# Kernel tuning notes

Hardware: AMD Instinct MI355X
Metric: run time of the kernel (lower is better)

## Reference

```python
import jax, jax.numpy as jnp
import numpy as np

N_NODES = 100000
N_EDGES = 3200000
IN_C, HID_C, OUT_C = 64, 128, 64


def gcn_conv(x, src, dst, W, b, n):
    """PyG GCNConv: h = x @ W; out[d] += norm(e) * h[s]; norm = deg^-1/2[s]*deg^-1/2[d].
    src/dst already include self-loops."""
    h = x @ W  # [N, out_c]
    deg = jax.ops.segment_sum(jnp.ones_like(dst, dtype=h.dtype), dst, num_segments=n)
    dinv = jnp.where(deg > 0, jax.lax.rsqrt(deg), 0.0)
    norm = dinv[src] * dinv[dst]  # [E]
    msg = h[src] * norm[:, None]  # [E, out_c] -- dominant memory traffic
    return jax.ops.segment_sum(msg, dst, num_segments=n) + b


def setup_inputs() -> dict:
    key = jax.random.key(0)
    k1, k2, k3, k4 = jax.random.split(key, 4)
    x = jax.random.normal(k1, (N_NODES, IN_C), dtype=jnp.float32)
    edge_index = jax.random.randint(k2, (2, N_EDGES), 0, N_NODES, dtype=jnp.int64)
    W1 = jax.random.normal(k3, (IN_C, HID_C), dtype=jnp.float32) / np.sqrt(IN_C)
    b1 = jnp.zeros((HID_C,), dtype=jnp.float32)
    W2 = jax.random.normal(k4, (HID_C, OUT_C), dtype=jnp.float32) / np.sqrt(HID_C)
    b2 = jnp.zeros((OUT_C,), dtype=jnp.float32)
    return {"x": x, "edge_index": edge_index, "W1": W1, "b1": b1, "W2": W2, "b2": b2}


def reference(x, edge_index, W1, b1, W2, b2):
    n = x.shape[0]
    loops = jnp.arange(n, dtype=edge_index.dtype)  # self-loops, as PyG GCNConv adds
    src = jnp.concatenate([edge_index[0], loops])
    dst = jnp.concatenate([edge_index[1], loops])
    h = gcn_conv(x, src, dst, W1, b1, n)
    h = jax.nn.relu(h)
    out = gcn_conv(h, src, dst, W2, b2, n)
    return out
```

## Files before the change

### kernel.cpp

```cpp
#include <hip/hip_runtime.h>
#include <math.h>


#define IN_C 64
#define HID_C 128
#define OUT_C 64
#define BSHIFT 9
#define BW (1 << BSHIFT)
#define NPB 512
#define CAP 24576
#define CH_MAX 6272

typedef __attribute__((ext_vector_type(8))) short bf16x8;
typedef __attribute__((ext_vector_type(4))) float f32x4;
typedef __attribute__((ext_vector_type(2))) float v2f;

__device__ __forceinline__ unsigned short f2bf(float f) {
  unsigned u = __float_as_uint(f);
  return (unsigned short)((u + 0x7FFF + ((u >> 16) & 1)) >> 16);
}
__device__ __forceinline__ v2f cvt2(unsigned u) {
  v2f r;
  r.x = __uint_as_float(u << 16);
  r.y = __uint_as_float(u & 0xFFFF0000u);
  return r;
}
__device__ __forceinline__ unsigned pack2(v2f v) {
  return ((unsigned)f2bf(v.y) << 16) | f2bf(v.x);
}


__global__ __launch_bounds__(256) void k_build(const int* __restrict__ ei, int e, int n,
    int nb, int* __restrict__ gcnt, unsigned* __restrict__ ebuf,
    const float* __restrict__ W1, const float* __restrict__ W2,
    unsigned short* __restrict__ Wt1, unsigned short* __restrict__ Wt2,
    unsigned short* __restrict__ xs_zero, unsigned short* __restrict__ h2s_zero) {
  const int t = threadIdx.x;
  if (blockIdx.x >= NPB) {
    int bb = blockIdx.x - NPB;
    if (bb == 32) {
      if (t < 64) { xs_zero[t] = 0; h2s_zero[t] = 0; }
      return;
    }
    int i = bb * 256 + t;
    if (i < IN_C * HID_C) {
      int k = i >> 7, c = i & (HID_C - 1);
      Wt1[c * IN_C + k] = f2bf(W1[i]);
    }
    if (i < HID_C * OUT_C) {
      int k = i >> 6, c = i & (OUT_C - 1);
      Wt2[c * HID_C + k] = f2bf(W2[i]);
    }
    return;
  }
  __shared__ unsigned lpay[CH_MAX];
  __shared__ unsigned char lbuck[CH_MAX];
  __shared__ int lh[256];
  __shared__ int lbase[256];
  __shared__ int lcur[256];
  __shared__ int sflag;
  if (t == 0) sflag = 0;
  __syncthreads();
  const int chunk = (e + NPB - 1) / NPB;
  const int lo = blockIdx.x * chunk;
  const int hi = min(lo + chunk, e);
  {
    int lim = min(hi, lo + 512);
    int f = 0;
    for (int i = lo + t; i < lim; i += 256)
      if (ei[2 * i + 1] != 0) f = 1;
    if (f) sflag = 1;
  }
  __syncthreads();
  const int f = sflag;
  for (int sub = lo; sub < hi; sub += CH_MAX) {
    const int shi = min(sub + CH_MAX, hi);
    const int mm = shi - sub;
    for (int i = t; i < nb; i += 256) lh[i] = 0;
    __syncthreads();
    for (int i = sub + t; i < shi; i += 256) {
      int s, d;
      if (f) {
        s = __builtin_nontemporal_load(&ei[i]);
        d = __builtin_nontemporal_load(&ei[e + i]);
      } else {
        s = (int)__builtin_nontemporal_load(&((const long long*)ei)[i]);
        d = (int)__builtin_nontemporal_load(&((const long long*)ei)[e + i]);
      }
      s = min(max(s, 0), n - 1);
      d = min(max(d, 0), n - 1);
      int bk = d >> BSHIFT;
      lpay[i - sub] = ((unsigned)(d & (BW - 1)) << 23) | (unsigned)s;
      lbuck[i - sub] = (unsigned char)bk;
      atomicAdd(&lh[bk], 1);
    }
    __syncthreads();
    for (int i = t; i < nb; i += 256) {
      int c = lh[i];
      lbase[i] = c ? atomicAdd(&gcnt[i], c) : 0;
      lcur[i] = 0;
    }
    __syncthreads();
    for (int i = t; i < mm; i += 256) {
      int bk = lbuck[i];
      int slot = lbase[bk] + atomicAdd(&lcur[bk], 1);
      if (slot < CAP) ebuf[(size_t)bk * CAP + slot] = lpay[i];
    }
    __syncthreads();
  }
}


__global__ __launch_bounds__(1024) void k_finalize(const unsigned* __restrict__ ebuf,
    const int* __restrict__ gcnt, const float* __restrict__ x,
    unsigned short* __restrict__ xs, int n, int nb,
    int* __restrict__ row_ptr, float* __restrict__ dinv, int* __restrict__ col) {
  __shared__ int sc[256];
  __shared__ int ldeg[BW];
  __shared__ int lofs[BW];
  __shared__ int lcur[BW];
  __shared__ float sdv[BW];
  __shared__ int wsum[256];
  const int b = blockIdx.x;
  const int t = threadIdx.x;
  const int T = 1024;
  int cnt = 0, nodes = 0;
  if (t < nb) {
    cnt = min(gcnt[t], CAP);
    nodes = min(BW, n - t * BW);
  }
  if (t < 256) sc[t] = cnt + nodes;
  __syncthreads();
  for (int off = 1; off < 256; off <<= 1) {
    int vc = 0;
    if (t < 256 && t >= off) vc = sc[t - off];
    __syncthreads();
    if (t < 256) sc[t] += vc;
    __syncthreads();
  }
  const int cntb = min(gcnt[b], CAP);
  const int eb = b * CAP;
  const int ee = eb + cntb;
  const int cb = (b == 0) ? 0 : sc[b - 1];
  const int lo = b * BW;
  const int nn = min(BW, n - lo);
  for (int k = t; k < BW; k += T) ldeg[k] = 0;
  __syncthreads();
  for (int k = t; k < nn; k += T) ldeg[k] = 1;
  __syncthreads();
  for (int j = eb + t; j < ee; j += T) {
    int dl = (int)(ebuf[j] >> 23);
    atomicAdd(&ldeg[dl], 1);
  }
  __syncthreads();
  int p0 = 0, p1 = 0;
  if (t < 256) {
    p0 = ldeg[2 * t]; p1 = ldeg[2 * t + 1];
    wsum[t] = p0 + p1;
  }
  __syncthreads();
  for (int off = 1; off < 256; off <<= 1) {
    int v = 0;
    if (t < 256 && t >= off) v = wsum[t - off];
    __syncthreads();
    if (t < 256) wsum[t] += v;
    __syncthreads();
  }
  if (t < 256) {
    int pb = (t == 0) ? 0 : wsum[t - 1];
    lofs[2 * t] = pb;
    lofs[2 * t + 1] = pb + p0;
  }
  __syncthreads();
  for (int k = t; k < nn; k += T) {
    int base = cb + lofs[k];
    float dv = rsqrtf((float)ldeg[k]);
    row_ptr[lo + k] = base;
    dinv[lo + k] = dv;
    sdv[k] = dv;
    col[base] = lo + k;
    lcur[k] = lofs[k] + 1;
  }
  if (b == nb - 1 && t == 0) row_ptr[n] = sc[nb - 1];
  __syncthreads();
  for (int j = eb + t; j < ee; j += T) {
    unsigned pk = ebuf[j];
    int s = (int)(pk & 0x7FFFFF);
    int dl = (int)(pk >> 23);
    int p = atomicAdd(&lcur[dl], 1);
    col[cb + p] = s;
  }
  const float4* x4 = (const float4*)x;
  for (int idx = t; idx < nn * 16; idx += T) {
    int row = idx >> 4, q = idx & 15;
    float sc2 = sdv[row];
    float4 v = x4[(size_t)(lo + row) * 16 + q];
    ushort4 o;
    o.x = f2bf(v.x * sc2); o.y = f2bf(v.y * sc2);
    o.z = f2bf(v.z * sc2); o.w = f2bf(v.w * sc2);
    ((ushort4*)xs)[(size_t)(lo + row) * 16 + q] = o;
  }
}


__device__ __forceinline__ void agg_row(const char* __restrict__ fb,
    const int* __restrict__ col, int beg, int end, int es, unsigned coff, int n,
    v2f& a0, v2f& a1, v2f& a2, v2f& a3) {
  const int rem = end - beg - es;
  const int c = (rem > 0) ? ((rem + 7) >> 3) : 0;
  const int last = end - 1;
  const unsigned zrow = ((unsigned)n << 7) | coff;
  for (int g = 0; g < c; g += 4) {
    int j0 = beg + es + 8 * g;
    int i0 = __builtin_nontemporal_load(&col[j0]);
    int i1 = __builtin_nontemporal_load(&col[min(j0 + 8, last)]);
    int i2 = __builtin_nontemporal_load(&col[min(j0 + 16, last)]);
    int i3 = __builtin_nontemporal_load(&col[min(j0 + 24, last)]);
    unsigned o0 = ((unsigned)i0 << 7) | coff;
    unsigned o1 = (g + 1 >= c) ? zrow : (((unsigned)i1 << 7) | coff);
    unsigned o2 = (g + 2 >= c) ? zrow : (((unsigned)i2 << 7) | coff);
    unsigned o3 = (g + 3 >= c) ? zrow : (((unsigned)i3 << 7) | coff);
    uint4 u0 = *(const uint4*)(fb + o0);
    uint4 u1 = *(const uint4*)(fb + o1);
    uint4 u2 = *(const uint4*)(fb + o2);
    uint4 u3 = *(const uint4*)(fb + o3);
    a0 += cvt2(u0.x) + cvt2(u1.x) + cvt2(u2.x) + cvt2(u3.x);
    a1 += cvt2(u0.y) + cvt2(u1.y) + cvt2(u2.y) + cvt2(u3.y);
    a2 += cvt2(u0.z) + cvt2(u1.z) + cvt2(u2.z) + cvt2(u3.z);
    a3 += cvt2(u0.w) + cvt2(u1.w) + cvt2(u2.w) + cvt2(u3.w);
  }
#pragma unroll
  for (int off = 8; off <= 32; off <<= 1) {
    v2f o0, o1, o2, o3;
    o0.x = __shfl_xor(a0.x, off); o0.y = __shfl_xor(a0.y, off);
    o1.x = __shfl_xor(a1.x, off); o1.y = __shfl_xor(a1.y, off);
    o2.x = __shfl_xor(a2.x, off); o2.y = __shfl_xor(a2.y, off);
    o3.x = __shfl_xor(a3.x, off); o3.y = __shfl_xor(a3.y, off);
    a0 += o0; a1 += o1; a2 += o2; a3 += o3;
  }
}


__global__ __launch_bounds__(256) void k_agg2(const unsigned short* __restrict__ feat,
    const int* __restrict__ row_ptr, const int* __restrict__ col,
    const float* __restrict__ dinv, const float* __restrict__ bias,
    float* __restrict__ out, int n) {
  const int wid = threadIdx.x >> 6;
  const int lane = threadIdx.x & 63;
  const int es = lane >> 3;
  const int c8 = lane & 7;
  const int d = blockIdx.x * 4 + wid;
  if (d >= n) return;
  const int beg = row_ptr[d], end = row_ptr[d + 1];
  v2f a0 = {0.f, 0.f}, a1 = {0.f, 0.f}, a2 = {0.f, 0.f}, a3 = {0.f, 0.f};
  agg_row((const char*)feat, col, beg, end, es, (unsigned)c8 * 16u, n,
          a0, a1, a2, a3);
  if (es == 0) {
    float sc = dinv[d];
    v2f vs = {sc, sc};
    a0 *= vs; a1 *= vs; a2 *= vs; a3 *= vs;
    const v2f* b2v = (const v2f*)bias;
    a0 += b2v[c8 * 4 + 0]; a1 += b2v[c8 * 4 + 1];
    a2 += b2v[c8 * 4 + 2]; a3 += b2v[c8 * 4 + 3];
    float4* o4 = (float4*)out;
    o4[(size_t)d * 16 + c8 * 2]     = make_float4(a0.x, a0.y, a1.x, a1.y);
    o4[(size_t)d * 16 + c8 * 2 + 1] = make_float4(a2.x, a2.y, a3.x, a3.y);
  }
}


__global__ __launch_bounds__(512) void k_aggmlp(const unsigned short* __restrict__ feat,
    const int* __restrict__ row_ptr, const int* __restrict__ col,
    const float* __restrict__ dinv, const float* __restrict__ b1,
    const unsigned short* __restrict__ Wt1, const unsigned short* __restrict__ Wt2,
    unsigned short* __restrict__ h2s, int n) {
  __shared__ __align__(16) unsigned short sA1[16][72];
  __shared__ __align__(16) unsigned short sH[16][136];
  const int wv = threadIdx.x >> 6;
  const int lane = threadIdx.x & 63;
  const int es = lane >> 3;
  const int c8 = lane & 7;
  const int r0 = blockIdx.x * 16;
  const unsigned coff = (unsigned)c8 * 16u;
  for (int rr = 0; rr < 2; ++rr) {
    const int d = r0 + wv * 2 + rr;
    if (d < n) {
      const int beg = row_ptr[d], end = row_ptr[d + 1];
      v2f a0 = {0.f, 0.f}, a1 = {0.f, 0.f}, a2 = {0.f, 0.f}, a3 = {0.f, 0.f};
      agg_row((const char*)feat, col, beg, end, es, coff, n, a0, a1, a2, a3);
      if (es == 0) {
        float sc = dinv[d];
        v2f vs = {sc, sc};
        a0 *= vs; a1 *= vs; a2 *= vs; a3 *= vs;
        uint4 o;
        o.x = pack2(a0); o.y = pack2(a1); o.z = pack2(a2); o.w = pack2(a3);
        *(uint4*)&sA1[wv * 2 + rr][c8 * 8] = o;
      }
    } else if (es == 0) {
      uint4 z = {0u, 0u, 0u, 0u};
      *(uint4*)&sA1[wv * 2 + rr][c8 * 8] = z;
    }
  }
  __syncthreads();
  const int m = lane & 15;
  const int q = lane >> 4;
  f32x4 acc0 = {0.f, 0.f, 0.f, 0.f};
#pragma unroll
  for (int kt = 0; kt < IN_C; kt += 32) {
    bf16x8 a = *(const bf16x8*)&sA1[m][kt + q * 8];
    bf16x8 p = *(const bf16x8*)&Wt1[(size_t)(wv * 16 + m) * IN_C + kt + q * 8];
    acc0 = __builtin_amdgcn_mfma_f32_16x16x32_bf16(a, p, acc0, 0, 0, 0);
  }
  float dv[4];
#pragma unroll
  for (int i = 0; i < 4; i++) dv[i] = dinv[min(r0 + q * 4 + i, n - 1)];
  {
    int c = wv * 16 + m;
    float bv = b1[c];
#pragma unroll
    for (int i = 0; i < 4; i++)
      sH[q * 4 + i][c] = f2bf(fmaxf(acc0[i] + bv, 0.f) * dv[i]);
  }
  __syncthreads();
  if (wv < 4) {
    f32x4 acc = {0.f, 0.f, 0.f, 0.f};
#pragma unroll
    for (int kt = 0; kt < HID_C; kt += 32) {
      bf16x8 a = *(const bf16x8*)&sH[m][kt + q * 8];
      bf16x8 p = *(const bf16x8*)&Wt2[(size_t)(wv * 16 + m) * HID_C + kt + q * 8];
      acc = __builtin_amdgcn_mfma_f32_16x16x32_bf16(a, p, acc, 0, 0, 0);
    }
    int c = wv * 16 + m;
#pragma unroll
    for (int i = 0; i < 4; i++) {
      int row = r0 + q * 4 + i;
      if (row < n) h2s[(size_t)row * OUT_C + c] = f2bf(acc[i]);
    }
  }
}


extern "C" void kernel_launch(void* const* d_in, const int* in_sizes, int n_in,
                              void* d_out, int out_size, void* d_ws, size_t ws_size,
                              hipStream_t stream) {
  const float* x  = (const float*)d_in[0];
  const int*   ei = (const int*)d_in[1];
  const float* W1 = (const float*)d_in[2];
  const float* b1 = (const float*)d_in[3];
  const float* W2 = (const float*)d_in[4];
  const float* b2 = (const float*)d_in[5];
  float* out = (float*)d_out;

  const int n = in_sizes[0] / IN_C;
  const int e = in_sizes[1] / 2;
  const int nb = (n + BW - 1) >> BSHIFT;

  char* p = (char*)d_ws;
  auto alloc = [&](size_t bytes) {
    char* r = p;
    p += (bytes + 255) & ~(size_t)255;
    return r;
  };
  int*   gcnt       = (int*)alloc((size_t)nb * 4);
  int*   row_ptr    = (int*)alloc((size_t)(n + 1) * 4);
  float* dinv       = (float*)alloc((size_t)n * 4);
  int*   col        = (int*)alloc((size_t)(e + n) * 4);
  unsigned* ebuf    = (unsigned*)alloc((size_t)nb * CAP * 4);
  unsigned short* xs  = (unsigned short*)alloc((size_t)(n + 1) * IN_C * 2);
  unsigned short* h2s = (unsigned short*)alloc((size_t)(n + 1) * OUT_C * 2);
  unsigned short* Wt1 = (unsigned short*)alloc((size_t)IN_C * HID_C * 2);
  unsigned short* Wt2 = (unsigned short*)alloc((size_t)HID_C * OUT_C * 2);

  hipMemsetAsync(gcnt, 0, (size_t)nb * 4, stream);

  k_build<<<NPB + 33, 256, 0, stream>>>(ei, e, n, nb, gcnt, ebuf, W1, W2, Wt1, Wt2,
      xs + (size_t)n * IN_C, h2s + (size_t)n * OUT_C);
  k_finalize<<<nb, 1024, 0, stream>>>(ebuf, gcnt, x, xs, n, nb, row_ptr, dinv, col);

  k_aggmlp<<<(n + 15) / 16, 512, 0, stream>>>(xs, row_ptr, col, dinv, b1, Wt1, Wt2, h2s, n);
  k_agg2<<<(n + 3) / 4, 256, 0, stream>>>(h2s, row_ptr, col, dinv, b2, out, n);
}
```

Measured before the change: 290.4 us.

## Merge all stages into one persistent cooperative kernel with grid syncs

Replaces the four separate kernels (build, finalize, aggregate+MLP, aggregate) with a single persistent kernel, launched cooperatively, that uses grid-wide syncs between phases. Layer-1 aggregation now writes an intermediate A1 buffer and a separate phase runs the MLP on 64-row tiles. This aims to remove launch gaps and tail effects between kernels. In exchange it adds grid barriers, an extra global round trip for A1, fewer resident threads per phase, and a multi-launch fallback when cooperative launch is unavailable.

```diff
diff --git a/kernel.cpp b/kernel.cpp
--- a/kernel.cpp
+++ b/kernel.cpp
@@ -1,5 +1,8 @@
 #include <hip/hip_runtime.h>
+#include <hip/hip_cooperative_groups.h>
 #include <math.h>
+
+namespace cg = cooperative_groups;
 
 
 #define IN_C 64
@@ -7,9 +10,11 @@
 #define OUT_C 64
 #define BSHIFT 9
 #define BW (1 << BSHIFT)
-#define NPB 512
+#define MAXBLK 512
+#define NTHR 1024
 #define CAP 24576
 #define CH_MAX 6272
+#define SMEM_BYTES 35840
 
 typedef __attribute__((ext_vector_type(8))) short bf16x8;
 typedef __attribute__((ext_vector_type(4))) float f32x4;
@@ -27,179 +32,6 @@
 }
 __device__ __forceinline__ unsigned pack2(v2f v) {
   return ((unsigned)f2bf(v.y) << 16) | f2bf(v.x);
-}
-
-
-__global__ __launch_bounds__(256) void k_build(const int* __restrict__ ei, int e, int n,
-    int nb, int* __restrict__ gcnt, unsigned* __restrict__ ebuf,
-    const float* __restrict__ W1, const float* __restrict__ W2,
-    unsigned short* __restrict__ Wt1, unsigned short* __restrict__ Wt2,
-    unsigned short* __restrict__ xs_zero, unsigned short* __restrict__ h2s_zero) {
-  const int t = threadIdx.x;
-  if (blockIdx.x >= NPB) {
-    int bb = blockIdx.x - NPB;
-    if (bb == 32) {
-      if (t < 64) { xs_zero[t] = 0; h2s_zero[t] = 0; }
-      return;
-    }
-    int i = bb * 256 + t;
-    if (i < IN_C * HID_C) {
-      int k = i >> 7, c = i & (HID_C - 1);
-      Wt1[c * IN_C + k] = f2bf(W1[i]);
-    }
-    if (i < HID_C * OUT_C) {
-      int k = i >> 6, c = i & (OUT_C - 1);
-      Wt2[c * HID_C + k] = f2bf(W2[i]);
-    }
-    return;
-  }
-  __shared__ unsigned lpay[CH_MAX];
-  __shared__ unsigned char lbuck[CH_MAX];
-  __shared__ int lh[256];
-  __shared__ int lbase[256];
-  __shared__ int lcur[256];
-  __shared__ int sflag;
-  if (t == 0) sflag = 0;
-  __syncthreads();
-  const int chunk = (e + NPB - 1) / NPB;
-  const int lo = blockIdx.x * chunk;
-  const int hi = min(lo + chunk, e);
-  {
-    int lim = min(hi, lo + 512);
-    int f = 0;
-    for (int i = lo + t; i < lim; i += 256)
-      if (ei[2 * i + 1] != 0) f = 1;
-    if (f) sflag = 1;
-  }
-  __syncthreads();
-  const int f = sflag;
-  for (int sub = lo; sub < hi; sub += CH_MAX) {
-    const int shi = min(sub + CH_MAX, hi);
-    const int mm = shi - sub;
-    for (int i = t; i < nb; i += 256) lh[i] = 0;
-    __syncthreads();
-    for (int i = sub + t; i < shi; i += 256) {
-      int s, d;
-      if (f) {
-        s = __builtin_nontemporal_load(&ei[i]);
-        d = __builtin_nontemporal_load(&ei[e + i]);
-      } else {
-        s = (int)__builtin_nontemporal_load(&((const long long*)ei)[i]);
-        d = (int)__builtin_nontemporal_load(&((const long long*)ei)[e + i]);
-      }
-      s = min(max(s, 0), n - 1);
-      d = min(max(d, 0), n - 1);
-      int bk = d >> BSHIFT;
-      lpay[i - sub] = ((unsigned)(d & (BW - 1)) << 23) | (unsigned)s;
-      lbuck[i - sub] = (unsigned char)bk;
-      atomicAdd(&lh[bk], 1);
-    }
-    __syncthreads();
-    for (int i = t; i < nb; i += 256) {
-      int c = lh[i];
-      lbase[i] = c ? atomicAdd(&gcnt[i], c) : 0;
-      lcur[i] = 0;
-    }
-    __syncthreads();
-    for (int i = t; i < mm; i += 256) {
-      int bk = lbuck[i];
-      int slot = lbase[bk] + atomicAdd(&lcur[bk], 1);
-      if (slot < CAP) ebuf[(size_t)bk * CAP + slot] = lpay[i];
-    }
-    __syncthreads();
-  }
-}
-
-
-__global__ __launch_bounds__(1024) void k_finalize(const unsigned* __restrict__ ebuf,
-    const int* __restrict__ gcnt, const float* __restrict__ x,
-    unsigned short* __restrict__ xs, int n, int nb,
-    int* __restrict__ row_ptr, float* __restrict__ dinv, int* __restrict__ col) {
-  __shared__ int sc[256];
-  __shared__ int ldeg[BW];
-  __shared__ int lofs[BW];
-  __shared__ int lcur[BW];
-  __shared__ float sdv[BW];
-  __shared__ int wsum[256];
-  const int b = blockIdx.x;
-  const int t = threadIdx.x;
-  const int T = 1024;
-  int cnt = 0, nodes = 0;
-  if (t < nb) {
-    cnt = min(gcnt[t], CAP);
-    nodes = min(BW, n - t * BW);
-  }
-  if (t < 256) sc[t] = cnt + nodes;
-  __syncthreads();
-  for (int off = 1; off < 256; off <<= 1) {
-    int vc = 0;
-    if (t < 256 && t >= off) vc = sc[t - off];
-    __syncthreads();
-    if (t < 256) sc[t] += vc;
-    __syncthreads();
-  }
-  const int cntb = min(gcnt[b], CAP);
-  const int eb = b * CAP;
-  const int ee = eb + cntb;
-  const int cb = (b == 0) ? 0 : sc[b - 1];
-  const int lo = b * BW;
-  const int nn = min(BW, n - lo);
-  for (int k = t; k < BW; k += T) ldeg[k] = 0;
-  __syncthreads();
-  for (int k = t; k < nn; k += T) ldeg[k] = 1;
-  __syncthreads();
-  for (int j = eb + t; j < ee; j += T) {
-    int dl = (int)(ebuf[j] >> 23);
-    atomicAdd(&ldeg[dl], 1);
-  }
-  __syncthreads();
-  int p0 = 0, p1 = 0;
-  if (t < 256) {
-    p0 = ldeg[2 * t]; p1 = ldeg[2 * t + 1];
-    wsum[t] = p0 + p1;
-  }
-  __syncthreads();
-  for (int off = 1; off < 256; off <<= 1) {
-    int v = 0;
-    if (t < 256 && t >= off) v = wsum[t - off];
-    __syncthreads();
-    if (t < 256) wsum[t] += v;
-    __syncthreads();
-  }
-  if (t < 256) {
-    int pb = (t == 0) ? 0 : wsum[t - 1];
-    lofs[2 * t] = pb;
-    lofs[2 * t + 1] = pb + p0;
-  }
-  __syncthreads();
-  for (int k = t; k < nn; k += T) {
-    int base = cb + lofs[k];
-    float dv = rsqrtf((float)ldeg[k]);
-    row_ptr[lo + k] = base;
-    dinv[lo + k] = dv;
-    sdv[k] = dv;
-    col[base] = lo + k;
-    lcur[k] = lofs[k] + 1;
-  }
-  if (b == nb - 1 && t == 0) row_ptr[n] = sc[nb - 1];
-  __syncthreads();
-  for (int j = eb + t; j < ee; j += T) {
-    unsigned pk = ebuf[j];
-    int s = (int)(pk & 0x7FFFFF);
-    int dl = (int)(pk >> 23);
-    int p = atomicAdd(&lcur[dl], 1);
-    col[cb + p] = s;
-  }
-  const float4* x4 = (const float4*)x;
-  for (int idx = t; idx < nn * 16; idx += T) {
-    int row = idx >> 4, q = idx & 15;
-    float sc2 = sdv[row];
-    float4 v = x4[(size_t)(lo + row) * 16 + q];
-    ushort4 o;
-    o.x = f2bf(v.x * sc2); o.y = f2bf(v.y * sc2);
-    o.z = f2bf(v.z * sc2); o.w = f2bf(v.w * sc2);
-    ((ushort4*)xs)[(size_t)(lo + row) * 16 + q] = o;
-  }
 }
 
 
@@ -216,10 +48,10 @@
     int i1 = __builtin_nontemporal_load(&col[min(j0 + 8, last)]);
     int i2 = __builtin_nontemporal_load(&col[min(j0 + 16, last)]);
     int i3 = __builtin_nontemporal_load(&col[min(j0 + 24, last)]);
-    unsigned o0 = ((unsigned)i0 << 7) | coff;
-    unsigned o1 = (g + 1 >= c) ? zrow : (((unsigned)i1 << 7) | coff);
-    unsigned o2 = (g + 2 >= c) ? zrow : (((unsigned)i2 << 7) | coff);
-    unsigned o3 = (g + 3 >= c) ? zrow : (((unsigned)i3 << 7) | coff);
+    unsigned o0 = min(((unsigned)i0 << 7) | coff, zrow);
+    unsigned o1 = (g + 1 >= c) ? zrow : min(((unsigned)i1 << 7) | coff, zrow);
+    unsigned o2 = (g + 2 >= c) ? zrow : min(((unsigned)i2 << 7) | coff, zrow);
+    unsigned o3 = (g + 3 >= c) ? zrow : min(((unsigned)i3 << 7) | coff, zrow);
     uint4 u0 = *(const uint4*)(fb + o0);
     uint4 u1 = *(const uint4*)(fb + o1);
     uint4 u2 = *(const uint4*)(fb + o2);
@@ -241,100 +73,291 @@
 }
 
 
-__global__ __launch_bounds__(256) void k_agg2(const unsigned short* __restrict__ feat,
-    const int* __restrict__ row_ptr, const int* __restrict__ col,
-    const float* __restrict__ dinv, const float* __restrict__ bias,
-    float* __restrict__ out, int n) {
-  const int wid = threadIdx.x >> 6;
-  const int lane = threadIdx.x & 63;
-  const int es = lane >> 3;
-  const int c8 = lane & 7;
-  const int d = blockIdx.x * 4 + wid;
-  if (d >= n) return;
-  const int beg = row_ptr[d], end = row_ptr[d + 1];
-  v2f a0 = {0.f, 0.f}, a1 = {0.f, 0.f}, a2 = {0.f, 0.f}, a3 = {0.f, 0.f};
-  agg_row((const char*)feat, col, beg, end, es, (unsigned)c8 * 16u, n,
-          a0, a1, a2, a3);
-  if (es == 0) {
-    float sc = dinv[d];
-    v2f vs = {sc, sc};
-    a0 *= vs; a1 *= vs; a2 *= vs; a3 *= vs;
-    const v2f* b2v = (const v2f*)bias;
-    a0 += b2v[c8 * 4 + 0]; a1 += b2v[c8 * 4 + 1];
-    a2 += b2v[c8 * 4 + 2]; a3 += b2v[c8 * 4 + 3];
-    float4* o4 = (float4*)out;
-    o4[(size_t)d * 16 + c8 * 2]     = make_float4(a0.x, a0.y, a1.x, a1.y);
-    o4[(size_t)d * 16 + c8 * 2 + 1] = make_float4(a2.x, a2.y, a3.x, a3.y);
-  }
-}
-
-
-__global__ __launch_bounds__(512) void k_aggmlp(const unsigned short* __restrict__ feat,
-    const int* __restrict__ row_ptr, const int* __restrict__ col,
-    const float* __restrict__ dinv, const float* __restrict__ b1,
-    const unsigned short* __restrict__ Wt1, const unsigned short* __restrict__ Wt2,
-    unsigned short* __restrict__ h2s, int n) {
-  __shared__ __align__(16) unsigned short sA1[16][72];
-  __shared__ __align__(16) unsigned short sH[16][136];
-  const int wv = threadIdx.x >> 6;
-  const int lane = threadIdx.x & 63;
-  const int es = lane >> 3;
-  const int c8 = lane & 7;
-  const int r0 = blockIdx.x * 16;
-  const unsigned coff = (unsigned)c8 * 16u;
-  for (int rr = 0; rr < 2; ++rr) {
-    const int d = r0 + wv * 2 + rr;
-    if (d < n) {
-      const int beg = row_ptr[d], end = row_ptr[d + 1];
+__global__ __launch_bounds__(NTHR, 8) void k_all(
+    const float* __restrict__ x, const int* __restrict__ ei,
+    const float* __restrict__ W1, const float* __restrict__ b1v,
+    const float* __restrict__ W2, const float* __restrict__ b2v,
+    float* __restrict__ out, int e, int n, int nb,
+    int* __restrict__ gcnt, unsigned* __restrict__ ebuf,
+    int* __restrict__ row_ptr, float* __restrict__ dinv,
+    int* __restrict__ col, int col_cap,
+    unsigned short* __restrict__ xs, unsigned short* __restrict__ A1,
+    unsigned short* __restrict__ h2s,
+    unsigned short* __restrict__ Wt1, unsigned short* __restrict__ Wt2,
+    int plo, int phi, int coop) {
+  __shared__ __align__(16) char smem[SMEM_BYTES];
+  const int bid = blockIdx.x;
+  const int gd = gridDim.x;
+  const int t = threadIdx.x;
+
+  if (plo <= 0 && 0 < phi) {
+    if (bid == 0) {
+      for (int i = t; i < IN_C * HID_C; i += NTHR) {
+        int k = i >> 7, c = i & (HID_C - 1);
+        Wt1[c * IN_C + k] = f2bf(W1[i]);
+      }
+    } else if (bid == 1) {
+      for (int i = t; i < HID_C * OUT_C; i += NTHR) {
+        int k = i >> 6, c = i & (OUT_C - 1);
+        Wt2[c * HID_C + k] = f2bf(W2[i]);
+      }
+    } else if (bid == 2) {
+      if (t < IN_C) xs[(size_t)n * IN_C + t] = 0;
+      if (t < OUT_C) h2s[(size_t)n * OUT_C + t] = 0;
+    }
+  }
+
+  if (plo <= 1 && 1 < phi) {
+    unsigned* lpay = (unsigned*)smem;
+    unsigned char* lbuck = (unsigned char*)(lpay + CH_MAX);
+    int* lh = (int*)(lbuck + CH_MAX);
+    int* lbase = lh + 256;
+    int* lcur = lbase + 256;
+    int* sflag = lcur + 256;
+    if (t == 0) *sflag = 0;
+    for (int i = t; i < 256; i += NTHR) lh[i] = 0;
+    __syncthreads();
+    const int chunk = (e + gd - 1) / gd;
+    const int lo = bid * chunk;
+    const int hi = min(lo + chunk, e);
+    {
+      int lim = min(hi, lo + 1024);
+      int fl = 0;
+      for (int i = lo + t; i < lim; i += NTHR)
+        if (ei[2 * i + 1] != 0) fl = 1;
+      if (fl) *sflag = 1;
+    }
+    __syncthreads();
+    const int f = *sflag;
+    const int nsub = (chunk + CH_MAX - 1) / CH_MAX;
+    for (int su = 0; su < nsub; ++su) {
+      const int sub = lo + su * CH_MAX;
+      const int shi = min(sub + CH_MAX, hi);
+      const int mm = max(shi - sub, 0);
+      for (int i = sub + t; i < shi; i += NTHR) {
+        int s, d;
+        if (f) {
+          s = __builtin_nontemporal_load(&ei[i]);
+          d = __builtin_nontemporal_load(&ei[e + i]);
+        } else {
+          s = (int)__builtin_nontemporal_load(&((const long long*)ei)[i]);
+          d = (int)__builtin_nontemporal_load(&((const long long*)ei)[e + i]);
+        }
+        s = min(max(s, 0), n - 1);
+        d = min(max(d, 0), n - 1);
+        int bk = d >> BSHIFT;
+        lpay[i - sub] = ((unsigned)(d & (BW - 1)) << 23) | (unsigned)s;
+        lbuck[i - sub] = (unsigned char)bk;
+        atomicAdd(&lh[bk], 1);
+      }
+      __syncthreads();
+      for (int i = t; i < nb; i += NTHR) {
+        int c = lh[i];
+        lbase[i] = c ? atomicAdd(&gcnt[i], c) : 0;
+        lh[i] = 0;
+        lcur[i] = 0;
+      }
+      __syncthreads();
+      for (int i = t; i < mm; i += NTHR) {
+        int bk = lbuck[i];
+        int slot = lbase[bk] + atomicAdd(&lcur[bk], 1);
+        if (slot < CAP) ebuf[(size_t)bk * CAP + slot] = lpay[i];
+      }
+      __syncthreads();
+    }
+  }
+  if (coop && 2 < phi) cg::this_grid().sync();
+
+  if (plo <= 2 && 2 < phi && bid < nb) {
+    int* sc = (int*)smem;
+    int* ldeg = sc + 256;
+    int* lofs = ldeg + BW;
+    int* lcur = lofs + BW;
+    float* sdv = (float*)(lcur + BW);
+    int* wsum = (int*)(sdv + BW);
+    const int b = bid;
+    int pc = 0;
+    if (t < nb) {
+      int cnt = min(__hip_atomic_load(&gcnt[t], __ATOMIC_RELAXED, __HIP_MEMORY_SCOPE_AGENT), CAP);
+      int nodes = min(BW, n - t * BW);
+      pc = (cnt + nodes + 31) & ~31;
+    }
+    if (t < 256) sc[t] = pc;
+    __syncthreads();
+    for (int off = 1; off < 256; off <<= 1) {
+      int vc = 0;
+      if (t < 256 && t >= off) vc = sc[t - off];
+      __syncthreads();
+      if (t < 256) sc[t] += vc;
+      __syncthreads();
+    }
+    const int cntb = min(__hip_atomic_load(&gcnt[b], __ATOMIC_RELAXED, __HIP_MEMORY_SCOPE_AGENT), CAP);
+    const int eb = b * CAP;
+    const int ee = eb + cntb;
+    const int cb = (b == 0) ? 0 : sc[b - 1];
+    const int lo = b * BW;
+    const int nn = min(BW, n - lo);
+    for (int k = t; k < BW; k += NTHR) ldeg[k] = 0;
+    __syncthreads();
+    for (int k = t; k < nn; k += NTHR) ldeg[k] = 1;
+    __syncthreads();
+    for (int j = eb + t; j < ee; j += NTHR) {
+      unsigned pk = __hip_atomic_load(&ebuf[j], __ATOMIC_RELAXED, __HIP_MEMORY_SCOPE_AGENT);
+      atomicAdd(&ldeg[(int)(pk >> 23)], 1);
+    }
+    __syncthreads();
+    int p0 = 0, p1 = 0;
+    if (t < 256) {
+      p0 = ldeg[2 * t]; p1 = ldeg[2 * t + 1];
+      wsum[t] = p0 + p1;
+    }
+    __syncthreads();
+    for (int off = 1; off < 256; off <<= 1) {
+      int v = 0;
+      if (t < 256 && t >= off) v = wsum[t - off];
+      __syncthreads();
+      if (t < 256) wsum[t] += v;
+      __syncthreads();
+    }
+    if (t < 256) {
+      int pb = (t == 0) ? 0 : wsum[t - 1];
+      lofs[2 * t] = pb;
+      lofs[2 * t + 1] = pb + p0;
+    }
+    __syncthreads();
+    for (int k = t; k < nn; k += NTHR) {
+      int base = cb + lofs[k];
+      float dv = rsqrtf((float)ldeg[k]);
+      row_ptr[lo + k] = base;
+      dinv[lo + k] = dv;
+      sdv[k] = dv;
+      if (base >= 0 && base < col_cap) col[base] = lo + k;
+      lcur[k] = lofs[k] + 1;
+    }
+    if (b == nb - 1 && t == 0) row_ptr[n] = cb + cntb + nn;
+    __syncthreads();
+    for (int j = eb + t; j < ee; j += NTHR) {
+      unsigned pk = __hip_atomic_load(&ebuf[j], __ATOMIC_RELAXED, __HIP_MEMORY_SCOPE_AGENT);
+      int s = (int)(pk & 0x7FFFFF);
+      int dl = (int)(pk >> 23);
+      int p = atomicAdd(&lcur[dl], 1);
+      int idx = cb + p;
+      if (idx >= 0 && idx < col_cap) col[idx] = s;
+    }
+    const float4* x4 = (const float4*)x;
+    for (int idx = t; idx < nn * 16; idx += NTHR) {
+      int row = idx >> 4, q = idx & 15;
+      float sc2 = sdv[row];
+      float4 v = x4[(size_t)(lo + row) * 16 + q];
+      ushort4 o;
+      o.x = f2bf(v.x * sc2); o.y = f2bf(v.y * sc2);
+      o.z = f2bf(v.z * sc2); o.w = f2bf(v.w * sc2);
+      ((ushort4*)xs)[(size_t)(lo + row) * 16 + q] = o;
+    }
+  }
+  if (coop && 3 < phi) cg::this_grid().sync();
+
+  if (plo <= 3 && 3 < phi) {
+    const int wv = t >> 6;
+    const int lane = t & 63;
+    const int es = lane >> 3;
+    const int c8 = lane & 7;
+    const unsigned coff = (unsigned)c8 * 16u;
+    for (int d = bid * 16 + wv; d < n; d += gd * 16) {
+      int beg = row_ptr[d], end = row_ptr[d + 1];
+      beg = max(beg, 0); end = min(end, col_cap); end = max(end, beg);
       v2f a0 = {0.f, 0.f}, a1 = {0.f, 0.f}, a2 = {0.f, 0.f}, a3 = {0.f, 0.f};
-      agg_row((const char*)feat, col, beg, end, es, coff, n, a0, a1, a2, a3);
+      agg_row((const char*)xs, col, beg, end, es, coff, n, a0, a1, a2, a3);
       if (es == 0) {
-        float sc = dinv[d];
-        v2f vs = {sc, sc};
+        float scv = dinv[d];
+        v2f vs = {scv, scv};
         a0 *= vs; a1 *= vs; a2 *= vs; a3 *= vs;
         uint4 o;
         o.x = pack2(a0); o.y = pack2(a1); o.z = pack2(a2); o.w = pack2(a3);
-        *(uint4*)&sA1[wv * 2 + rr][c8 * 8] = o;
-      }
-    } else if (es == 0) {
-      uint4 z = {0u, 0u, 0u, 0u};
-      *(uint4*)&sA1[wv * 2 + rr][c8 * 8] = z;
-    }
-  }
-  __syncthreads();
-  const int m = lane & 15;
-  const int q = lane >> 4;
-  f32x4 acc0 = {0.f, 0.f, 0.f, 0.f};
-#pragma unroll
-  for (int kt = 0; kt < IN_C; kt += 32) {
-    bf16x8 a = *(const bf16x8*)&sA1[m][kt + q * 8];
-    bf16x8 p = *(const bf16x8*)&Wt1[(size_t)(wv * 16 + m) * IN_C + kt + q * 8];
-    acc0 = __builtin_amdgcn_mfma_f32_16x16x32_bf16(a, p, acc0, 0, 0, 0);
-  }
-  float dv[4];
-#pragma unroll
-  for (int i = 0; i < 4; i++) dv[i] = dinv[min(r0 + q * 4 + i, n - 1)];
-  {
-    int c = wv * 16 + m;
-    float bv = b1[c];
-#pragma unroll
-    for (int i = 0; i < 4; i++)
-      sH[q * 4 + i][c] = f2bf(fmaxf(acc0[i] + bv, 0.f) * dv[i]);
-  }
-  __syncthreads();
-  if (wv < 4) {
-    f32x4 acc = {0.f, 0.f, 0.f, 0.f};
-#pragma unroll
-    for (int kt = 0; kt < HID_C; kt += 32) {
-      bf16x8 a = *(const bf16x8*)&sH[m][kt + q * 8];
-      bf16x8 p = *(const bf16x8*)&Wt2[(size_t)(wv * 16 + m) * HID_C + kt + q * 8];
-      acc = __builtin_amdgcn_mfma_f32_16x16x32_bf16(a, p, acc, 0, 0, 0);
-    }
-    int c = wv * 16 + m;
-#pragma unroll
-    for (int i = 0; i < 4; i++) {
-      int row = r0 + q * 4 + i;
-      if (row < n) h2s[(size_t)row * OUT_C + c] = f2bf(acc[i]);
+        ((uint4*)A1)[(size_t)d * 8 + c8] = o;
+      }
+    }
+  }
+  if (coop && 4 < phi) cg::this_grid().sync();
+
+  if (plo <= 4 && 4 < phi) {
+    typedef unsigned short ush;
+    ush (*sH)[136] = (ush(*)[136])smem;
+    const int wv = t >> 6;
+    const int team = wv >> 2;
+    const int tw = wv & 3;
+    const int lane = t & 63;
+    const int m = lane & 15;
+    const int q = lane >> 4;
+    const int nt64 = (n + 63) >> 6;
+    for (int tile = bid; tile < nt64; tile += gd) {
+      const int r0t = tile * 64 + team * 16;
+      const int ra = min(r0t + m, n - 1);
+      f32x4 acc0 = {0.f, 0.f, 0.f, 0.f}, acc1 = {0.f, 0.f, 0.f, 0.f};
+#pragma unroll
+      for (int kt = 0; kt < IN_C; kt += 32) {
+        bf16x8 a  = *(const bf16x8*)&A1[(size_t)ra * IN_C + kt + q * 8];
+        bf16x8 p  = *(const bf16x8*)&Wt1[(size_t)(tw * 16 + m) * IN_C + kt + q * 8];
+        bf16x8 p2 = *(const bf16x8*)&Wt1[(size_t)((tw + 4) * 16 + m) * IN_C + kt + q * 8];
+        acc0 = __builtin_amdgcn_mfma_f32_16x16x32_bf16(a, p, acc0, 0, 0, 0);
+        acc1 = __builtin_amdgcn_mfma_f32_16x16x32_bf16(a, p2, acc1, 0, 0, 0);
+      }
+      float dv[4];
+#pragma unroll
+      for (int i = 0; i < 4; i++) dv[i] = dinv[min(r0t + q * 4 + i, n - 1)];
+      {
+        int c = tw * 16 + m;
+        float bv = b1v[c];
+#pragma unroll
+        for (int i = 0; i < 4; i++)
+          sH[team * 16 + q * 4 + i][c] = f2bf(fmaxf(acc0[i] + bv, 0.f) * dv[i]);
+        c = (tw + 4) * 16 + m;
+        bv = b1v[c];
+#pragma unroll
+        for (int i = 0; i < 4; i++)
+          sH[team * 16 + q * 4 + i][c] = f2bf(fmaxf(acc1[i] + bv, 0.f) * dv[i]);
+      }
+      __syncthreads();
+      f32x4 acc = {0.f, 0.f, 0.f, 0.f};
+#pragma unroll
+      for (int kt = 0; kt < HID_C; kt += 32) {
+        bf16x8 a = *(const bf16x8*)&sH[team * 16 + m][kt + q * 8];
+        bf16x8 p = *(const bf16x8*)&Wt2[(size_t)(tw * 16 + m) * HID_C + kt + q * 8];
+        acc = __builtin_amdgcn_mfma_f32_16x16x32_bf16(a, p, acc, 0, 0, 0);
+      }
+      int c = tw * 16 + m;
+#pragma unroll
+      for (int i = 0; i < 4; i++) {
+        int row = r0t + q * 4 + i;
+        if (row < n) h2s[(size_t)row * OUT_C + c] = f2bf(acc[i]);
+      }
+      __syncthreads();
+    }
+  }
+  if (coop && 5 < phi) cg::this_grid().sync();
+
+  if (plo <= 5 && 5 < phi) {
+    const int wv = t >> 6;
+    const int lane = t & 63;
+    const int es = lane >> 3;
+    const int c8 = lane & 7;
+    const unsigned coff = (unsigned)c8 * 16u;
+    const v2f* b2p = (const v2f*)b2v;
+    for (int d = bid * 16 + wv; d < n; d += gd * 16) {
+      int beg = row_ptr[d], end = row_ptr[d + 1];
+      beg = max(beg, 0); end = min(end, col_cap); end = max(end, beg);
+      v2f a0 = {0.f, 0.f}, a1 = {0.f, 0.f}, a2 = {0.f, 0.f}, a3 = {0.f, 0.f};
+      agg_row((const char*)h2s, col, beg, end, es, coff, n, a0, a1, a2, a3);
+      if (es == 0) {
+        float scv = dinv[d];
+        v2f vs = {scv, scv};
+        a0 *= vs; a1 *= vs; a2 *= vs; a3 *= vs;
+        a0 += b2p[c8 * 4 + 0]; a1 += b2p[c8 * 4 + 1];
+        a2 += b2p[c8 * 4 + 2]; a3 += b2p[c8 * 4 + 3];
+        float4* o4 = (float4*)out;
+        o4[(size_t)d * 16 + c8 * 2]     = make_float4(a0.x, a0.y, a1.x, a1.y);
+        o4[(size_t)d * 16 + c8 * 2 + 1] = make_float4(a2.x, a2.y, a3.x, a3.y);
+      }
     }
   }
 }
@@ -355,28 +378,63 @@
   const int e = in_sizes[1] / 2;
   const int nb = (n + BW - 1) >> BSHIFT;
 
+  static int s_nblk = -1;
+  static int s_coop = 0;
+  if (s_nblk < 0) {
+    int dev = 0;
+    hipGetDevice(&dev);
+    hipDeviceProp_t props;
+    hipGetDeviceProperties(&props, dev);
+    int maxb = 0;
+    hipOccupancyMaxActiveBlocksPerMultiprocessor(&maxb, (const void*)k_all, NTHR, 0);
+    if (maxb < 1) maxb = 1;
+    long cap = (long)maxb * props.multiProcessorCount;
+    s_nblk = (int)(cap < MAXBLK ? cap : MAXBLK);
+    if (s_nblk < 1) s_nblk = 256;
+    s_coop = props.cooperativeLaunch ? 1 : 0;
+    if (s_nblk < nb) s_coop = 0;
+  }
+
   char* p = (char*)d_ws;
   auto alloc = [&](size_t bytes) {
     char* r = p;
     p += (bytes + 255) & ~(size_t)255;
     return r;
   };
-  int*   gcnt       = (int*)alloc((size_t)nb * 4);
+  const int col_cap = e + n + 32 * nb + 64;
+  int*   gcnt       = (int*)alloc((size_t)256 * 4);
   int*   row_ptr    = (int*)alloc((size_t)(n + 1) * 4);
   float* dinv       = (float*)alloc((size_t)n * 4);
-  int*   col        = (int*)alloc((size_t)(e + n) * 4);
+  int*   col        = (int*)alloc((size_t)col_cap * 4);
   unsigned* ebuf    = (unsigned*)alloc((size_t)nb * CAP * 4);
   unsigned short* xs  = (unsigned short*)alloc((size_t)(n + 1) * IN_C * 2);
+  unsigned short* A1  = (unsigned short*)alloc((size_t)n * IN_C * 2);
   unsigned short* h2s = (unsigned short*)alloc((size_t)(n + 1) * OUT_C * 2);
   unsigned short* Wt1 = (unsigned short*)alloc((size_t)IN_C * HID_C * 2);
   unsigned short* Wt2 = (unsigned short*)alloc((size_t)HID_C * OUT_C * 2);
 
-  hipMemsetAsync(gcnt, 0, (size_t)nb * 4, stream);
-
-  k_build<<<NPB + 33, 256, 0, stream>>>(ei, e, n, nb, gcnt, ebuf, W1, W2, Wt1, Wt2,
-      xs + (size_t)n * IN_C, h2s + (size_t)n * OUT_C);
-  k_finalize<<<nb, 1024, 0, stream>>>(ebuf, gcnt, x, xs, n, nb, row_ptr, dinv, col);
-
-  k_aggmlp<<<(n + 15) / 16, 512, 0, stream>>>(xs, row_ptr, col, dinv, b1, Wt1, Wt2, h2s, n);
-  k_agg2<<<(n + 3) / 4, 256, 0, stream>>>(h2s, row_ptr, col, dinv, b2, out, n);
-}
+  hipMemsetAsync(gcnt, 0, (size_t)256 * 4, stream);
+
+  if (s_coop) {
+    int plo = 0, phi = 6, coop = 1;
+    void* args[] = {
+      (void*)&x, (void*)&ei, (void*)&W1, (void*)&b1, (void*)&W2, (void*)&b2,
+      (void*)&out, (void*)&e, (void*)&n, (void*)&nb,
+      (void*)&gcnt, (void*)&ebuf, (void*)&row_ptr, (void*)&dinv,
+      (void*)&col, (void*)&col_cap, (void*)&xs, (void*)&A1, (void*)&h2s,
+      (void*)&Wt1, (void*)&Wt2, (void*)&plo, (void*)&phi, (void*)&coop};
+    hipLaunchCooperativeKernel((const void*)k_all, dim3(s_nblk), dim3(NTHR),
+                               args, 0, stream);
+  } else {
+    k_all<<<s_nblk, NTHR, 0, stream>>>(x, ei, W1, b1, W2, b2, out, e, n, nb,
+        gcnt, ebuf, row_ptr, dinv, col, col_cap, xs, A1, h2s, Wt1, Wt2, 0, 2, 0);
+    k_all<<<s_nblk, NTHR, 0, stream>>>(x, ei, W1, b1, W2, b2, out, e, n, nb,
+        gcnt, ebuf, row_ptr, dinv, col, col_cap, xs, A1, h2s, Wt1, Wt2, 2, 3, 0);
+    k_all<<<s_nblk, NTHR, 0, stream>>>(x, ei, W1, b1, W2, b2, out, e, n, nb,
+        gcnt, ebuf, row_ptr, dinv, col, col_cap, xs, A1, h2s, Wt1, Wt2, 3, 4, 0);
+    k_all<<<s_nblk, NTHR, 0, stream>>>(x, ei, W1, b1, W2, b2, out, e, n, nb,
+        gcnt, ebuf, row_ptr, dinv, col, col_cap, xs, A1, h2s, Wt1, Wt2, 4, 5, 0);
+    k_all<<<s_nblk, NTHR, 0, stream>>>(x, ei, W1, b1, W2, b2, out, e, n, nb,
+        gcnt, ebuf, row_ptr, dinv, col, col_cap, xs, A1, h2s, Wt1, Wt2, 5, 6, 0);
+  }
+}
```

Measured after the change: 478.8 us. 64.9% more time.

## Split fused aggregate+MLP kernel into separate aggregation and MLP kernels

Applied to the files above, without the earlier changes.

Replaces the fused k_aggmlp kernel with three stages. A templated aggregation kernel writes layer-1 aggregated features to a bf16 buffer A1. A standalone MFMA MLP kernel then reads A1 and computes both matmuls with 256 threads, each wave handling two hidden column tiles. Finally, the shared aggregation kernel handles layer 2. Splitting out the gather is meant to give it higher occupancy without the shared-memory and sync overhead of the fused block, at the cost of an extra round trip of about 12.8MB through A1. It also widens k_build to 1024 threads per block and collapses the weight-transpose blocks into one looping block.

```diff
diff --git a/kernel.cpp b/kernel.cpp
--- a/kernel.cpp
+++ b/kernel.cpp
@@ -30,26 +30,27 @@
 }
 
 
-__global__ __launch_bounds__(256) void k_build(const int* __restrict__ ei, int e, int n,
+__global__ __launch_bounds__(1024) void k_build(const int* __restrict__ ei, int e, int n,
     int nb, int* __restrict__ gcnt, unsigned* __restrict__ ebuf,
     const float* __restrict__ W1, const float* __restrict__ W2,
     unsigned short* __restrict__ Wt1, unsigned short* __restrict__ Wt2,
     unsigned short* __restrict__ xs_zero, unsigned short* __restrict__ h2s_zero) {
   const int t = threadIdx.x;
+  const int T = 1024;
   if (blockIdx.x >= NPB) {
     int bb = blockIdx.x - NPB;
-    if (bb == 32) {
-      if (t < 64) { xs_zero[t] = 0; h2s_zero[t] = 0; }
-      return;
-    }
-    int i = bb * 256 + t;
-    if (i < IN_C * HID_C) {
-      int k = i >> 7, c = i & (HID_C - 1);
-      Wt1[c * IN_C + k] = f2bf(W1[i]);
-    }
-    if (i < HID_C * OUT_C) {
-      int k = i >> 6, c = i & (OUT_C - 1);
-      Wt2[c * HID_C + k] = f2bf(W2[i]);
+    if (bb == 0) {
+      for (int i = t; i < IN_C * HID_C; i += T) {
+        int k = i >> 7, c = i & (HID_C - 1);
+        Wt1[c * IN_C + k] = f2bf(W1[i]);
+      }
+      for (int i = t; i < HID_C * OUT_C; i += T) {
+        int k = i >> 6, c = i & (OUT_C - 1);
+        Wt2[c * HID_C + k] = f2bf(W2[i]);
+      }
+    } else {
+      if (t < IN_C) xs_zero[t] = 0;
+      if (t < OUT_C) h2s_zero[t] = 0;
     }
     return;
   }
@@ -65,9 +66,9 @@
   const int lo = blockIdx.x * chunk;
   const int hi = min(lo + chunk, e);
   {
-    int lim = min(hi, lo + 512);
+    int lim = min(hi, lo + 1024);
     int f = 0;
-    for (int i = lo + t; i < lim; i += 256)
+    for (int i = lo + t; i < lim; i += T)
       if (ei[2 * i + 1] != 0) f = 1;
     if (f) sflag = 1;
   }
@@ -76,9 +77,9 @@
   for (int sub = lo; sub < hi; sub += CH_MAX) {
     const int shi = min(sub + CH_MAX, hi);
     const int mm = shi - sub;
-    for (int i = t; i < nb; i += 256) lh[i] = 0;
-    __syncthreads();
-    for (int i = sub + t; i < shi; i += 256) {
+    for (int i = t; i < nb; i += T) lh[i] = 0;
+    __syncthreads();
+    for (int i = sub + t; i < shi; i += T) {
       int s, d;
       if (f) {
         s = __builtin_nontemporal_load(&ei[i]);
@@ -95,13 +96,13 @@
       atomicAdd(&lh[bk], 1);
     }
     __syncthreads();
-    for (int i = t; i < nb; i += 256) {
+    for (int i = t; i < nb; i += T) {
       int c = lh[i];
       lbase[i] = c ? atomicAdd(&gcnt[i], c) : 0;
       lcur[i] = 0;
     }
     __syncthreads();
-    for (int i = t; i < mm; i += 256) {
+    for (int i = t; i < mm; i += T) {
       int bk = lbuck[i];
       int slot = lbase[bk] + atomicAdd(&lcur[bk], 1);
       if (slot < CAP) ebuf[(size_t)bk * CAP + slot] = lpay[i];
@@ -241,10 +242,11 @@
 }
 
 
-__global__ __launch_bounds__(256) void k_agg2(const unsigned short* __restrict__ feat,
+template<bool BIAS, bool OUT_BF16>
+__global__ __launch_bounds__(256) void k_agg(const unsigned short* __restrict__ feat,
     const int* __restrict__ row_ptr, const int* __restrict__ col,
     const float* __restrict__ dinv, const float* __restrict__ bias,
-    float* __restrict__ out, int n) {
+    void* __restrict__ outv, int n) {
   const int wid = threadIdx.x >> 6;
   const int lane = threadIdx.x & 63;
   const int es = lane >> 3;
@@ -259,83 +261,72 @@
     float sc = dinv[d];
     v2f vs = {sc, sc};
     a0 *= vs; a1 *= vs; a2 *= vs; a3 *= vs;
-    const v2f* b2v = (const v2f*)bias;
-    a0 += b2v[c8 * 4 + 0]; a1 += b2v[c8 * 4 + 1];
-    a2 += b2v[c8 * 4 + 2]; a3 += b2v[c8 * 4 + 3];
-    float4* o4 = (float4*)out;
-    o4[(size_t)d * 16 + c8 * 2]     = make_float4(a0.x, a0.y, a1.x, a1.y);
-    o4[(size_t)d * 16 + c8 * 2 + 1] = make_float4(a2.x, a2.y, a3.x, a3.y);
-  }
-}
-
-
-__global__ __launch_bounds__(512) void k_aggmlp(const unsigned short* __restrict__ feat,
-    const int* __restrict__ row_ptr, const int* __restrict__ col,
-    const float* __restrict__ dinv, const float* __restrict__ b1,
+    if (BIAS) {
+      const v2f* b2v = (const v2f*)bias;
+      a0 += b2v[c8 * 4 + 0]; a1 += b2v[c8 * 4 + 1];
+      a2 += b2v[c8 * 4 + 2]; a3 += b2v[c8 * 4 + 3];
+    }
+    if (OUT_BF16) {
+      uint4 o;
+      o.x = pack2(a0); o.y = pack2(a1); o.z = pack2(a2); o.w = pack2(a3);
+      ((uint4*)outv)[(size_t)d * 8 + c8] = o;
+    } else {
+      float4* o4 = (float4*)outv;
+      o4[(size_t)d * 16 + c8 * 2]     = make_float4(a0.x, a0.y, a1.x, a1.y);
+      o4[(size_t)d * 16 + c8 * 2 + 1] = make_float4(a2.x, a2.y, a3.x, a3.y);
+    }
+  }
+}
+
+
+__global__ __launch_bounds__(256) void k_mlp(const unsigned short* __restrict__ A1,
     const unsigned short* __restrict__ Wt1, const unsigned short* __restrict__ Wt2,
-    unsigned short* __restrict__ h2s, int n) {
-  __shared__ __align__(16) unsigned short sA1[16][72];
-  __shared__ __align__(16) unsigned short sH[16][136];
+    const float* __restrict__ b1, const float* __restrict__ dinv,
+    unsigned short* __restrict__ h2s, int M) {
+  __shared__ unsigned short sA[16 * 136];
   const int wv = threadIdx.x >> 6;
   const int lane = threadIdx.x & 63;
-  const int es = lane >> 3;
-  const int c8 = lane & 7;
-  const int r0 = blockIdx.x * 16;
-  const unsigned coff = (unsigned)c8 * 16u;
-  for (int rr = 0; rr < 2; ++rr) {
-    const int d = r0 + wv * 2 + rr;
-    if (d < n) {
-      const int beg = row_ptr[d], end = row_ptr[d + 1];
-      v2f a0 = {0.f, 0.f}, a1 = {0.f, 0.f}, a2 = {0.f, 0.f}, a3 = {0.f, 0.f};
-      agg_row((const char*)feat, col, beg, end, es, coff, n, a0, a1, a2, a3);
-      if (es == 0) {
-        float sc = dinv[d];
-        v2f vs = {sc, sc};
-        a0 *= vs; a1 *= vs; a2 *= vs; a3 *= vs;
-        uint4 o;
-        o.x = pack2(a0); o.y = pack2(a1); o.z = pack2(a2); o.w = pack2(a3);
-        *(uint4*)&sA1[wv * 2 + rr][c8 * 8] = o;
-      }
-    } else if (es == 0) {
-      uint4 z = {0u, 0u, 0u, 0u};
-      *(uint4*)&sA1[wv * 2 + rr][c8 * 8] = z;
-    }
-  }
-  __syncthreads();
   const int m = lane & 15;
   const int q = lane >> 4;
-  f32x4 acc0 = {0.f, 0.f, 0.f, 0.f};
+  const int r0 = blockIdx.x * 16;
+  const int ra = min(r0 + m, M - 1);
+  f32x4 acc0 = {0.f, 0.f, 0.f, 0.f}, acc1 = {0.f, 0.f, 0.f, 0.f};
 #pragma unroll
   for (int kt = 0; kt < IN_C; kt += 32) {
-    bf16x8 a = *(const bf16x8*)&sA1[m][kt + q * 8];
-    bf16x8 p = *(const bf16x8*)&Wt1[(size_t)(wv * 16 + m) * IN_C + kt + q * 8];
+    bf16x8 a  = *(const bf16x8*)&A1[(size_t)ra * IN_C + kt + q * 8];
+    bf16x8 p  = *(const bf16x8*)&Wt1[(size_t)(wv * 16 + m) * IN_C + kt + q * 8];
+    bf16x8 p2 = *(const bf16x8*)&Wt1[(size_t)((wv + 4) * 16 + m) * IN_C + kt + q * 8];
     acc0 = __builtin_amdgcn_mfma_f32_16x16x32_bf16(a, p, acc0, 0, 0, 0);
+    acc1 = __builtin_amdgcn_mfma_f32_16x16x32_bf16(a, p2, acc1, 0, 0, 0);
   }
   float dv[4];
 #pragma unroll
-  for (int i = 0; i < 4; i++) dv[i] = dinv[min(r0 + q * 4 + i, n - 1)];
+  for (int i = 0; i < 4; i++) dv[i] = dinv[min(r0 + q * 4 + i, M - 1)];
   {
     int c = wv * 16 + m;
     float bv = b1[c];
 #pragma unroll
     for (int i = 0; i < 4; i++)
-      sH[q * 4 + i][c] = f2bf(fmaxf(acc0[i] + bv, 0.f) * dv[i]);
-  }
-  __syncthreads();
-  if (wv < 4) {
-    f32x4 acc = {0.f, 0.f, 0.f, 0.f};
-#pragma unroll
-    for (int kt = 0; kt < HID_C; kt += 32) {
-      bf16x8 a = *(const bf16x8*)&sH[m][kt + q * 8];
-      bf16x8 p = *(const bf16x8*)&Wt2[(size_t)(wv * 16 + m) * HID_C + kt + q * 8];
-      acc = __builtin_amdgcn_mfma_f32_16x16x32_bf16(a, p, acc, 0, 0, 0);
-    }
-    int c = wv * 16 + m;
-#pragma unroll
-    for (int i = 0; i < 4; i++) {
-      int row = r0 + q * 4 + i;
-      if (row < n) h2s[(size_t)row * OUT_C + c] = f2bf(acc[i]);
-    }
+      sA[(q * 4 + i) * 136 + c] = f2bf(fmaxf(acc0[i] + bv, 0.f) * dv[i]);
+    c = (wv + 4) * 16 + m;
+    bv = b1[c];
+#pragma unroll
+    for (int i = 0; i < 4; i++)
+      sA[(q * 4 + i) * 136 + c] = f2bf(fmaxf(acc1[i] + bv, 0.f) * dv[i]);
+  }
+  __syncthreads();
+  f32x4 acc = {0.f, 0.f, 0.f, 0.f};
+#pragma unroll
+  for (int kt = 0; kt < HID_C; kt += 32) {
+    bf16x8 a = *(const bf16x8*)&sA[m * 136 + kt + q * 8];
+    bf16x8 p = *(const bf16x8*)&Wt2[(size_t)(wv * 16 + m) * HID_C + kt + q * 8];
+    acc = __builtin_amdgcn_mfma_f32_16x16x32_bf16(a, p, acc, 0, 0, 0);
+  }
+  int c = wv * 16 + m;
+#pragma unroll
+  for (int i = 0; i < 4; i++) {
+    int row = r0 + q * 4 + i;
+    if (row < M) h2s[(size_t)row * OUT_C + c] = f2bf(acc[i]);
   }
 }
 
@@ -367,16 +358,18 @@
   int*   col        = (int*)alloc((size_t)(e + n) * 4);
   unsigned* ebuf    = (unsigned*)alloc((size_t)nb * CAP * 4);
   unsigned short* xs  = (unsigned short*)alloc((size_t)(n + 1) * IN_C * 2);
+  unsigned short* A1  = (unsigned short*)alloc((size_t)n * IN_C * 2);
   unsigned short* h2s = (unsigned short*)alloc((size_t)(n + 1) * OUT_C * 2);
   unsigned short* Wt1 = (unsigned short*)alloc((size_t)IN_C * HID_C * 2);
   unsigned short* Wt2 = (unsigned short*)alloc((size_t)HID_C * OUT_C * 2);
 
   hipMemsetAsync(gcnt, 0, (size_t)nb * 4, stream);
 
-  k_build<<<NPB + 33, 256, 0, stream>>>(ei, e, n, nb, gcnt, ebuf, W1, W2, Wt1, Wt2,
+  k_build<<<NPB + 2, 1024, 0, stream>>>(ei, e, n, nb, gcnt, ebuf, W1, W2, Wt1, Wt2,
       xs + (size_t)n * IN_C, h2s + (size_t)n * OUT_C);
   k_finalize<<<nb, 1024, 0, stream>>>(ebuf, gcnt, x, xs, n, nb, row_ptr, dinv, col);
 
-  k_aggmlp<<<(n + 15) / 16, 512, 0, stream>>>(xs, row_ptr, col, dinv, b1, Wt1, Wt2, h2s, n);
-  k_agg2<<<(n + 3) / 4, 256, 0, stream>>>(h2s, row_ptr, col, dinv, b2, out, n);
-}
+  k_agg<false, true><<<(n + 3) / 4, 256, 0, stream>>>(xs, row_ptr, col, dinv, nullptr, A1, n);
+  k_mlp<<<(n + 15) / 16, 256, 0, stream>>>(A1, Wt1, Wt2, b1, dinv, h2s, n);
+  k_agg<true, false><<<(n + 3) / 4, 256, 0, stream>>>(h2s, row_ptr, col, dinv, b2, out, n);
+}
```

Result: slower. 302.1 us (+4.0%).
